# Kernel optimization log

Measured on AMD Instinct MI355X. Metric: run time of the kernel, lower is better.

## Reference

```python
import jax, jax.numpy as jnp
import numpy as np
from jax import lax

DIM = 384
HEADS = 8
HEAD_DIM = DIM // HEADS
EPS = 1e-06


def setup_inputs() -> dict:
    key = jax.random.key(0)
    ks = jax.random.split(key, 16)
    B, N, C = 8, 4096, DIM
    s = 0.02
    inp = {
        "x": jax.random.normal(ks[0], (B, N, C), jnp.float32),
        "wq": jax.random.normal(ks[1], (C, C), jnp.float32) * s,
        "bq": jnp.zeros((C,), jnp.float32),
        "wk": jax.random.normal(ks[2], (C, C), jnp.float32) * s,
        "bk": jnp.zeros((C,), jnp.float32),
        "wv": jax.random.normal(ks[3], (C, C), jnp.float32) * s,
        "bv": jnp.zeros((C,), jnp.float32),
        "wg": jax.random.normal(ks[4], (C, C), jnp.float32) * s,
        "bg": jnp.zeros((C,), jnp.float32),
        "wo": jax.random.normal(ks[5], (C, C), jnp.float32) * s,
        "bo": jnp.zeros((C,), jnp.float32),
        "temperature": jnp.ones((HEADS, 1, 1), jnp.float32),
        "dw_w": jax.random.normal(ks[6], (C, 1, 3, 3), jnp.float32) * s,  # depthwise 3x3
        "dw_b": jnp.zeros((C,), jnp.float32),
        "pw_w": jax.random.normal(ks[7], (C, C), jnp.float32) * s,        # pointwise 1x1
        "pw_b": jnp.zeros((C,), jnp.float32),
    }
    return inp


def _phi(x):
    # exp(x - max) over last dim, numerically stable
    return jnp.exp(x - jnp.max(x, axis=-1, keepdims=True))


def _token_mixer(x, dw_w, dw_b, pw_w, pw_b):
    B, N, C = x.shape
    H = W = int(np.sqrt(N))
    feat = x.transpose(0, 2, 1).reshape(B, C, H, W)
    feat = lax.conv_general_dilated(
        feat, dw_w, window_strides=(1, 1), padding=((1, 1), (1, 1)),
        feature_group_count=C, dimension_numbers=("NCHW", "OIHW", "NCHW"))
    feat = feat + dw_b[None, :, None, None]
    feat = jnp.einsum("bchw,oc->bohw", feat, pw_w) + pw_b[None, :, None, None]
    return feat.reshape(B, C, N).transpose(0, 2, 1)


def reference(x, wq, bq, wk, bk, wv, bv, wg, bg, wo, bo, temperature,
              dw_w, dw_b, pw_w, pw_b):
    B, N, C = x.shape
    residual = x
    x = x + _token_mixer(x, dw_w, dw_b, pw_w, pw_b)

    def heads(y):  # [B,N,C] -> [B,H,N,d]
        return y.reshape(B, N, HEADS, HEAD_DIM).transpose(0, 2, 1, 3)

    q = heads(jnp.einsum("bnc,oc->bno", x, wq) + bq)
    k = heads(jnp.einsum("bnc,oc->bno", x, wk) + bk)
    v = heads(jnp.einsum("bnc,oc->bno", x, wv) + bv)
    g = heads(jnp.einsum("bnc,oc->bno", x, wg) + bg)

    q = _phi(q * temperature[None])       # temperature: [H,1,1] broadcasts over [B,H,N,d]
    k = _phi(k)
    v = v * jax.nn.sigmoid(g)

    kv = jnp.einsum("bhnd,bhne->bhde", k, v)     # [B,H,d,d]
    k_sum = jnp.sum(k, axis=2)                   # [B,H,d]
    num = jnp.einsum("bhnd,bhde->bhne", q, kv)   # [B,H,N,d]
    den = jnp.einsum("bhnd,bhd->bhn", q, k_sum)[..., None] + EPS
    out = num / den

    out = out.transpose(0, 2, 1, 3).reshape(B, N, C)
    out = jnp.einsum("bnc,oc->bno", out, wo) + bo
    return out + 0.0 * residual
```

## Files before the change

kernel.cpp:

```cpp
#include <hip/hip_runtime.h>
#include <math.h>

#define EPSF 1e-6f

typedef __attribute__((ext_vector_type(8))) short bf16x8;
typedef __attribute__((ext_vector_type(4))) float f32x4;
typedef unsigned short u16;
typedef unsigned int u32;

#define MFMA16(a,b,c) __builtin_amdgcn_mfma_f32_16x16x32_bf16((a),(b),(c),0,0,0)

__device__ __forceinline__ u16 f2bf(float f){
  u32 x = __builtin_bit_cast(u32, f);
  u32 r = (x + 0x7fffu + ((x >> 16) & 1u)) >> 16;
  return (u16)r;
}
__device__ __forceinline__ void gll16(const void* g, void* l){
  __builtin_amdgcn_global_load_lds(
      (const __attribute__((address_space(1))) u32*)g,
      (__attribute__((address_space(3))) u32*)l, 16, 0, 0);
}

__global__ __launch_bounds__(256) void k01_prep_dw(
    const float* __restrict__ wq, const float* __restrict__ bq,
    const float* __restrict__ wk, const float* __restrict__ bk,
    const float* __restrict__ wv, const float* __restrict__ bv,
    const float* __restrict__ wg, const float* __restrict__ bg,
    const float* __restrict__ pw_w, const float* __restrict__ wo,
    u16* __restrict__ wpack, u16* __restrict__ pwb, u16* __restrict__ wob,
    float* __restrict__ bpack,
    const float* __restrict__ x, const float* __restrict__ dw_w,
    const float* __restrict__ dw_b, u16* __restrict__ t)
{
  if (blockIdx.x < 3456){
    int idx = blockIdx.x*256 + threadIdx.x;
    const int NW = 1536*384;
    if (idx < NW) {
      int r = idx / 384, c = idx - r*384;
      int h = r / 192, s = (r % 192)/48, d = r % 48;
      const float* w = (s==0)?wq:(s==1)?wk:(s==2)?wv:wg;
      wpack[idx] = f2bf(w[(h*48+d)*384 + c]);
      if (c==0){
        const float* b = (s==0)?bq:(s==1)?bk:(s==2)?bv:bg;
        bpack[r] = b[h*48+d];
      }
    } else if (idx < NW + 147456) {
      pwb[idx - NW] = f2bf(pw_w[idx - NW]);
    } else if (idx < NW + 2*147456) {
      wob[idx - NW - 147456] = f2bf(wo[idx - NW - 147456]);
    }
    return;
  }
  int idx = (blockIdx.x - 3456)*256 + threadIdx.x;
  int c4 = idx % 96; int rest = idx / 96;
  int jg = rest & 15; rest >>= 4;
  int i = rest & 63; int b = rest >> 6;
  int c0 = c4*4, j0 = jg*4;
  float wf[36];
  {
    const float4* wp = (const float4*)(dw_w + c0*9);
    #pragma unroll
    for (int k=0;k<9;k++){
      float4 v = wp[k];
      wf[4*k] = v.x; wf[4*k+1] = v.y; wf[4*k+2] = v.z; wf[4*k+3] = v.w;
    }
  }
  float4 bias = *(const float4*)(dw_b + c0);
  float acc[4][4];
  #pragma unroll
  for (int tk=0;tk<4;tk++){
    acc[tk][0]=bias.x; acc[tk][1]=bias.y; acc[tk][2]=bias.z; acc[tk][3]=bias.w;
  }
  const float* xb = x + ((size_t)b<<12)*384;
  #pragma unroll
  for (int di=-1; di<=1; ++di){
    int ii = i+di; if ((unsigned)ii >= 64u) continue;
    #pragma unroll
    for (int dj=-1; dj<=4; ++dj){
      int jj = j0+dj; if ((unsigned)jj >= 64u) continue;
      float4 xv = *(const float4*)(xb + (size_t)((ii<<6)+jj)*384 + c0);
      #pragma unroll
      for (int tk=0;tk<4;tk++){
        const int dd = dj - tk;
        if (dd < -1 || dd > 1) continue;
        const int tap = (di+1)*3 + (dd+1);
        acc[tk][0] = fmaf(xv.x, wf[0*9+tap], acc[tk][0]);
        acc[tk][1] = fmaf(xv.y, wf[1*9+tap], acc[tk][1]);
        acc[tk][2] = fmaf(xv.z, wf[2*9+tap], acc[tk][2]);
        acc[tk][3] = fmaf(xv.w, wf[3*9+tap], acc[tk][3]);
      }
    }
  }
  int mbase = (b<<12) + (i<<6) + j0;
  #pragma unroll
  for (int tk=0;tk<4;tk++){
    ushort4 o; o.x=f2bf(acc[tk][0]); o.y=f2bf(acc[tk][1]);
    o.z=f2bf(acc[tk][2]); o.w=f2bf(acc[tk][3]);
    *(ushort4*)(t + (size_t)(mbase+tk)*384 + c0) = o;
  }
}

__global__ __launch_bounds__(256) void k2_gemm_pw(
    const u16* __restrict__ t, const u16* __restrict__ pwb,
    const float* __restrict__ x, const float* __restrict__ pw_b,
    u16* __restrict__ xm)
{
  __shared__ __align__(16) u16 smem[32768];
  const int m0 = blockIdx.x * 128;
  const int n0 = blockIdx.y * 128;
  const int tid = threadIdx.x, w = tid>>6, l = tid&63;
  const int lc = l & 15, hi = l >> 4;
  const int osw = ((l&7) ^ (l>>3))*16;
  const f32x4 zf = {0.f,0.f,0.f,0.f};
  f32x4 acc[4][4];
  #pragma unroll
  for (int i=0;i<4;i++)
    #pragma unroll
    for (int j=0;j<4;j++) acc[i][j] = zf;

  const int srow = (w*4)*8 + (l>>3);

  #define K2_STAGE(T, BUF) do {                                            \
    const int k0_ = (T)*64;                                                \
    char* Ab_ = (char*)(smem + (BUF)*8192);                                \
    char* Bb_ = (char*)(smem + 16384 + (BUF)*8192);                        \
    _Pragma("unroll")                                                      \
    for (int i=0;i<4;i++){                                                 \
      gll16((const char*)t   + ((size_t)(m0+srow+i*8)*384 + k0_)*2 + osw,  \
            Ab_ + (w*4+i)*1024);                                           \
      gll16((const char*)pwb + ((size_t)(n0+srow+i*8)*384 + k0_)*2 + osw,  \
            Bb_ + (w*4+i)*1024);                                           \
    }                                                                      \
  } while(0)

  K2_STAGE(0, 0);
  __syncthreads();
  int cur = 0;
  for (int t_=0; t_<6; ++t_){
    if (t_ < 5) K2_STAGE(t_+1, cur^1);
    const u16* As = smem + cur*8192;
    const u16* Bs = smem + 16384 + cur*8192;
    const int wr = (w>>1)*64, wc = (w&1)*64;
    #pragma unroll
    for (int kk=0; kk<64; kk+=32){
      const int sc = (((kk>>3)+hi) ^ (lc&7))*8;
      bf16x8 a[4], bb[4];
      #pragma unroll
      for (int i=0;i<4;i++) a[i]  = *(const bf16x8*)&As[(wr + i*16 + lc)*64 + sc];
      #pragma unroll
      for (int j=0;j<4;j++) bb[j] = *(const bf16x8*)&Bs[(wc + j*16 + lc)*64 + sc];
      #pragma unroll
      for (int i=0;i<4;i++)
        #pragma unroll
        for (int j=0;j<4;j++)
          acc[i][j] = MFMA16(a[i], bb[j], acc[i][j]);
    }
    __syncthreads();
    cur ^= 1;
  }
  #undef K2_STAGE
  const int wr=(w>>1)*64, wc=(w&1)*64;
  #pragma unroll
  for (int j=0;j<4;j++){
    int n = n0 + wc + j*16 + lc;
    float bias = pw_b[n];
    #pragma unroll
    for (int i=0;i<4;i++)
      #pragma unroll
      for (int r=0;r<4;r++){
        int m = m0 + wr + i*16 + hi*4 + r;
        float v = acc[i][j][r] + x[(size_t)m*384 + n] + bias;
        xm[(size_t)m*384 + n] = f2bf(v);
      }
  }
}

__global__ __launch_bounds__(256) void k3_gemm_qkvg(
    const u16* __restrict__ xm, const u16* __restrict__ wpack,
    const float* __restrict__ bpack, const float* __restrict__ temperature,
    u16* __restrict__ qh, float* __restrict__ pkv, float* __restrict__ pks)
{
  __shared__ __align__(16) u16 smem[40960];
  const int m0 = blockIdx.y * 128;
  const int h  = blockIdx.x;
  const int tid = threadIdx.x, w = tid>>6, l = tid&63;
  const int lc = l & 15, hi = l >> 4;
  const int osw = ((l&7) ^ (l>>3))*16;
  const f32x4 zf = {0.f,0.f,0.f,0.f};
  f32x4 acc[2][12];
  #pragma unroll
  for (int i=0;i<2;i++)
    #pragma unroll
    for (int j=0;j<12;j++) acc[i][j] = zf;

  const int arow = (w*4)*8 + (l>>3);
  const int brow = (w*6)*8 + (l>>3);

  #define K3_STAGE(T, BUF) do {                                                \
    const int k0_ = (T)*64;                                                    \
    char* Ab_ = (char*)(smem + (BUF)*8192);                                    \
    char* Bb_ = (char*)(smem + 16384 + (BUF)*12288);                           \
    _Pragma("unroll")                                                          \
    for (int i=0;i<4;i++)                                                      \
      gll16((const char*)xm + ((size_t)(m0+arow+i*8)*384 + k0_)*2 + osw,       \
            Ab_ + (w*4+i)*1024);                                               \
    _Pragma("unroll")                                                          \
    for (int i=0;i<6;i++)                                                      \
      gll16((const char*)wpack + ((size_t)(h*192+brow+i*8)*384 + k0_)*2 + osw, \
            Bb_ + (w*6+i)*1024);                                               \
  } while(0)

  K3_STAGE(0, 0);
  __syncthreads();
  int cur = 0;
  const int rbase = w*32;
  for (int t=0; t<6; ++t){
    if (t < 5) K3_STAGE(t+1, cur^1);
    const u16* Ab = smem + cur*8192;
    const u16* Bb = smem + 16384 + cur*12288;
    #pragma unroll
    for (int kk=0; kk<64; kk+=32){
      const int sc = (((kk>>3)+hi) ^ (lc&7))*8;
      bf16x8 a0 = *(const bf16x8*)&Ab[(rbase +      lc)*64 + sc];
      bf16x8 a1 = *(const bf16x8*)&Ab[(rbase + 16 + lc)*64 + sc];
      #pragma unroll
      for (int j=0;j<12;j++){
        bf16x8 bb = *(const bf16x8*)&Bb[(j*16 + lc)*64 + sc];
        acc[0][j] = MFMA16(a0, bb, acc[0][j]);
        acc[1][j] = MFMA16(a1, bb, acc[1][j]);
      }
    }
    __syncthreads();
    cur ^= 1;
  }
  #undef K3_STAGE

  const float tq = temperature[h];
  const int b = m0 >> 12;
  const int mtile = (m0 >> 7) & 31;
  const size_t bh = (size_t)b*8 + h;
  const int bb0 = h*192;
  float biasq[3], biask[3], biasv[3], biasg[3];
  #pragma unroll
  for (int j=0;j<3;j++){
    biasq[j] = bpack[bb0       + j*16 + lc];
    biask[j] = bpack[bb0 + 48  + j*16 + lc];
    biasv[j] = bpack[bb0 + 96  + j*16 + lc];
    biasg[j] = bpack[bb0 + 144 + j*16 + lc];
  }
  u16* kT = smem;
  u16* vT = smem + 6528;
  float ksp[3] = {0.f, 0.f, 0.f};

  #pragma unroll
  for (int i=0;i<2;i++){
    ushort4 kst[3], vst[3];
    #pragma unroll
    for (int r=0;r<4;r++){
      int m = m0 + w*32 + i*16 + hi*4 + r;
      int n = m & 4095;
      size_t rowq = (bh*4096 + n)*48;
      float q0=(acc[i][0][r]+biasq[0])*tq;
      float q1=(acc[i][1][r]+biasq[1])*tq;
      float q2=(acc[i][2][r]+biasq[2])*tq;
      qh[rowq +      lc] = f2bf(__expf(q0));
      qh[rowq + 16 + lc] = f2bf(__expf(q1));
      qh[rowq + 32 + lc] = f2bf(__expf(q2));
      float s0=acc[i][3][r]+biask[0];
      float s1=acc[i][4][r]+biask[1];
      float s2=acc[i][5][r]+biask[2];
      float mk = fmaxf(s0,fmaxf(s1,s2));
      mk = fmaxf(mk, __shfl_xor(mk,1,64));
      mk = fmaxf(mk, __shfl_xor(mk,2,64));
      mk = fmaxf(mk, __shfl_xor(mk,4,64));
      mk = fmaxf(mk, __shfl_xor(mk,8,64));
      float k0e = __expf(s0-mk), k1e = __expf(s1-mk), k2e = __expf(s2-mk);
      ksp[0] += k0e; ksp[1] += k1e; ksp[2] += k2e;
      u16 kq0=f2bf(k0e), kq1=f2bf(k1e), kq2=f2bf(k2e);
      u16 vq[3];
      #pragma unroll
      for (int j=0;j<3;j++){
        float vv = acc[i][6+j][r] + biasv[j];
        float gg = acc[i][9+j][r] + biasg[j];
        float sg = __builtin_amdgcn_rcpf(1.f + __expf(-gg));
        vq[j] = f2bf(vv*sg);
      }
      if (r==0){ kst[0].x=kq0; kst[1].x=kq1; kst[2].x=kq2; vst[0].x=vq[0]; vst[1].x=vq[1]; vst[2].x=vq[2]; }
      if (r==1){ kst[0].y=kq0; kst[1].y=kq1; kst[2].y=kq2; vst[0].y=vq[0]; vst[1].y=vq[1]; vst[2].y=vq[2]; }
      if (r==2){ kst[0].z=kq0; kst[1].z=kq1; kst[2].z=kq2; vst[0].z=vq[0]; vst[1].z=vq[1]; vst[2].z=vq[2]; }
      if (r==3){ kst[0].w=kq0; kst[1].w=kq1; kst[2].w=kq2; vst[0].w=vq[0]; vst[1].w=vq[1]; vst[2].w=vq[2]; }
    }
    int mb = w*32 + i*16 + hi*4;
    #pragma unroll
    for (int j=0;j<3;j++){
      *(ushort4*)&kT[(j*16+lc)*136 + mb] = kst[j];
      *(ushort4*)&vT[(j*16+lc)*136 + mb] = vst[j];
    }
  }
  __syncthreads();

  bf16x8 af[3], bfv[3];
  #pragma unroll
  for (int da=0;da<3;da++) af[da]  = *(const bf16x8*)&kT[(da*16+lc)*136 + w*32 + hi*8];
  #pragma unroll
  for (int eb=0;eb<3;eb++) bfv[eb] = *(const bf16x8*)&vT[(eb*16+lc)*136 + w*32 + hi*8];
  f32x4 a2[3][3];
  #pragma unroll
  for (int da=0;da<3;da++)
    #pragma unroll
    for (int eb=0;eb<3;eb++)
      a2[da][eb] = MFMA16(af[da], bfv[eb], zf);
  __syncthreads();
  float* pb = (float*)smem + w*2304;
  #pragma unroll
  for (int da=0;da<3;da++)
    #pragma unroll
    for (int eb=0;eb<3;eb++)
      #pragma unroll
      for (int rr=0;rr<4;rr++)
        pb[(da*16 + hi*4 + rr)*48 + eb*16 + lc] = a2[da][eb][rr];
  __syncthreads();
  {
    float* p0 = (float*)smem;
    float* dst = pkv + ((size_t)bh*32 + mtile)*2304;
    for (int u=tid; u<2304; u+=256)
      dst[u] = p0[u] + p0[2304+u] + p0[4608+u] + p0[6912+u];
  }
  #pragma unroll
  for (int j=0;j<3;j++){
    ksp[j] += __shfl_xor(ksp[j],16,64);
    ksp[j] += __shfl_xor(ksp[j],32,64);
  }
  __syncthreads();
  {
    float* kr = (float*)smem;
    if (hi==0){ kr[w*48+lc]=ksp[0]; kr[w*48+16+lc]=ksp[1]; kr[w*48+32+lc]=ksp[2]; }
    __syncthreads();
    if (tid < 48){
      float* ds = pks + ((size_t)bh*32 + mtile)*48;
      ds[tid] = kr[tid] + kr[48+tid] + kr[96+tid] + kr[144+tid];
    }
  }
}

__global__ __launch_bounds__(256) void k5_red(
    const float* __restrict__ pkv, const float* __restrict__ pks,
    u16* __restrict__ kvp)
{
  __shared__ float sm[2304];
  __shared__ float ks[48];
  int bh = blockIdx.x, tid = threadIdx.x;
  const float* base = pkv + (size_t)bh*32*2304;
  for (int u=tid; u<2304; u+=256){
    float v = 0.f;
    #pragma unroll
    for (int m=0;m<32;m++) v += base[(size_t)m*2304 + u];
    sm[u] = v;
  }
  if (tid < 48){
    const float* bk = pks + (size_t)bh*32*48 + tid;
    float v = 0.f;
    #pragma unroll
    for (int m=0;m<32;m++) v += bk[m*48];
    ks[tid] = v;
  }
  __syncthreads();
  for (int u=tid; u<4096; u+=256){
    int e = u >> 6, d = u & 63;
    float v = 0.f;
    if (e < 48 && d < 48)       v = sm[d*48 + e];
    else if (e == 48 && d < 48) v = ks[d];
    kvp[((size_t)bh*64 + e)*64 + d] = f2bf(v);
  }
}

__global__ __launch_bounds__(256) void k6_num(
    const u16* __restrict__ qh, const u16* __restrict__ kvp, u16* __restrict__ ah)
{
  __shared__ __align__(16) u16 As[256*64];
  __shared__ __align__(16) u16 Bs[64*64];
  const int bh = blockIdx.x >> 4, nc = blockIdx.x & 15;
  const int tid = threadIdx.x, w = tid>>6, l = tid&63;
  const int lc = l & 15, hi = l >> 4;
  const f32x4 zf = {0.f,0.f,0.f,0.f};
  const uint4 z4 = {0,0,0,0};
  const u16* gq = qh + ((size_t)bh*4096 + nc*256)*48;
  #pragma unroll
  for (int it=0; it<8; ++it){
    int s = it*256 + tid;
    int row = s>>3, c = s&7, g = c ^ (row&7);
    ((uint4*)As)[s] = (g < 6) ? *(const uint4*)(gq + (size_t)row*48 + g*8) : z4;
  }
  const u16* gk = kvp + (size_t)bh*4096;
  #pragma unroll
  for (int it=0; it<2; ++it){
    int s = it*256 + tid;
    int row = s>>3, c = s&7, g = c ^ (row&7);
    ((uint4*)Bs)[s] = *(const uint4*)(gk + (size_t)row*64 + g*8);
  }
  __syncthreads();
  f32x4 acc[4][4];
  #pragma unroll
  for (int i=0;i<4;i++)
    #pragma unroll
    for (int j=0;j<4;j++) acc[i][j] = zf;
  const int rbase = w*64;
  #pragma unroll
  for (int kk=0; kk<64; kk+=32){
    const int sc = (((kk>>3)+hi) ^ (lc&7))*8;
    bf16x8 a[4], bb[4];
    #pragma unroll
    for (int i=0;i<4;i++) a[i]  = *(const bf16x8*)&As[(rbase + i*16 + lc)*64 + sc];
    #pragma unroll
    for (int j=0;j<4;j++) bb[j] = *(const bf16x8*)&Bs[(j*16 + lc)*64 + sc];
    #pragma unroll
    for (int i=0;i<4;i++)
      #pragma unroll
      for (int j=0;j<4;j++)
        acc[i][j] = MFMA16(a[i], bb[j], acc[i][j]);
  }
  const int b = bh >> 3, h = bh & 7;
  #pragma unroll
  for (int i=0;i<4;i++){
    #pragma unroll
    for (int r=0;r<4;r++){
      float den = __shfl(acc[i][3][r], l & 48, 64) + EPSF;
      float rd = __builtin_amdgcn_rcpf(den);
      int n = nc*256 + rbase + i*16 + hi*4 + r;
      size_t ob = ((size_t)b*4096 + n)*384 + h*48;
      ah[ob +      lc] = f2bf(acc[i][0][r]*rd);
      ah[ob + 16 + lc] = f2bf(acc[i][1][r]*rd);
      ah[ob + 32 + lc] = f2bf(acc[i][2][r]*rd);
    }
  }
}

__global__ __launch_bounds__(256) void k7_gemm_out(
    const u16* __restrict__ ah, const u16* __restrict__ wob,
    const float* __restrict__ bo, float* __restrict__ out)
{
  __shared__ __align__(16) u16 smem[32768];
  const int m0 = blockIdx.x * 128;
  const int n0 = blockIdx.y * 128;
  const int tid = threadIdx.x, w = tid>>6, l = tid&63;
  const int lc = l & 15, hi = l >> 4;
  const int osw = ((l&7) ^ (l>>3))*16;
  const f32x4 zf = {0.f,0.f,0.f,0.f};
  f32x4 acc[4][4];
  #pragma unroll
  for (int i=0;i<4;i++)
    #pragma unroll
    for (int j=0;j<4;j++) acc[i][j] = zf;

  const int srow = (w*4)*8 + (l>>3);

  #define K7_STAGE(T, BUF) do {                                            \
    const int k0_ = (T)*64;                                                \
    char* Ab_ = (char*)(smem + (BUF)*8192);                                \
    char* Bb_ = (char*)(smem + 16384 + (BUF)*8192);                        \
    _Pragma("unroll")                                                      \
    for (int i=0;i<4;i++){                                                 \
      gll16((const char*)ah  + ((size_t)(m0+srow+i*8)*384 + k0_)*2 + osw,  \
            Ab_ + (w*4+i)*1024);                                           \
      gll16((const char*)wob + ((size_t)(n0+srow+i*8)*384 + k0_)*2 + osw,  \
            Bb_ + (w*4+i)*1024);                                           \
    }                                                                      \
  } while(0)

  K7_STAGE(0, 0);
  __syncthreads();
  int cur = 0;
  for (int t_=0; t_<6; ++t_){
    if (t_ < 5) K7_STAGE(t_+1, cur^1);
    const u16* As = smem + cur*8192;
    const u16* Bs = smem + 16384 + cur*8192;
    const int wr = (w>>1)*64, wc = (w&1)*64;
    #pragma unroll
    for (int kk=0; kk<64; kk+=32){
      const int sc = (((kk>>3)+hi) ^ (lc&7))*8;
      bf16x8 a[4], bb[4];
      #pragma unroll
      for (int i=0;i<4;i++) a[i]  = *(const bf16x8*)&As[(wr + i*16 + lc)*64 + sc];
      #pragma unroll
      for (int j=0;j<4;j++) bb[j] = *(const bf16x8*)&Bs[(wc + j*16 + lc)*64 + sc];
      #pragma unroll
      for (int i=0;i<4;i++)
        #pragma unroll
        for (int j=0;j<4;j++)
          acc[i][j] = MFMA16(a[i], bb[j], acc[i][j]);
    }
    __syncthreads();
    cur ^= 1;
  }
  #undef K7_STAGE
  const int wr=(w>>1)*64, wc=(w&1)*64;
  #pragma unroll
  for (int j=0;j<4;j++){
    int n = n0 + wc + j*16 + lc;
    float bias = bo[n];
    #pragma unroll
    for (int i=0;i<4;i++)
      #pragma unroll
      for (int r=0;r<4;r++){
        int m = m0 + wr + i*16 + hi*4 + r;
        out[(size_t)m*384 + n] = acc[i][j][r] + bias;
      }
  }
}

extern "C" void kernel_launch(void* const* d_in, const int* in_sizes, int n_in,
                              void* d_out, int out_size, void* d_ws, size_t ws_size,
                              hipStream_t stream)
{
  const float* x    = (const float*)d_in[0];
  const float* wq   = (const float*)d_in[1];
  const float* bq   = (const float*)d_in[2];
  const float* wk   = (const float*)d_in[3];
  const float* bk   = (const float*)d_in[4];
  const float* wv   = (const float*)d_in[5];
  const float* bv   = (const float*)d_in[6];
  const float* wg   = (const float*)d_in[7];
  const float* bg   = (const float*)d_in[8];
  const float* wo   = (const float*)d_in[9];
  const float* bo   = (const float*)d_in[10];
  const float* temp = (const float*)d_in[11];
  const float* dw_w = (const float*)d_in[12];
  const float* dw_b = (const float*)d_in[13];
  const float* pw_w = (const float*)d_in[14];
  const float* pw_b = (const float*)d_in[15];
  float* out = (float*)d_out;
  char* ws = (char*)d_ws;

  u16*   t       = (u16*)(ws + 0);
  float* pkv     = (float*)(ws + 0);
  float* pks     = (float*)(ws + 18874368);
  u16*   ah      = (u16*)(ws + 0);
  u16*   xm      = (u16*)(ws + 25165824);
  u16*   qh      = (u16*)(ws + 50331648);
  u16*   wpack   = (u16*)(ws + 83886080);
  u16*   pwb     = (u16*)(ws + 85065728);
  u16*   wob     = (u16*)(ws + 85360640);
  float* bpack   = (float*)(ws + 85655552);
  u16*   kvp     = (u16*)(ws + 85661696);

  k01_prep_dw<<<6528, 256, 0, stream>>>(wq,bq,wk,bk,wv,bv,wg,bg,pw_w,wo,
                                        wpack,pwb,wob,bpack,
                                        x, dw_w, dw_b, t);
  k2_gemm_pw<<<dim3(256,3), 256, 0, stream>>>(t, pwb, x, pw_b, xm);
  k3_gemm_qkvg<<<dim3(8,256), 256, 0, stream>>>(xm, wpack, bpack, temp, qh, pkv, pks);
  k5_red<<<64, 256, 0, stream>>>(pkv, pks, kvp);
  k6_num<<<1024, 256, 0, stream>>>(qh, kvp, ah);
  k7_gemm_out<<<dim3(256,3), 256, 0, stream>>>(ah, wob, bo, out);
}
```

Measured before the change: 174.4 us.

## Store attention output head-major via LDS staging and swap k3 grid order

Result: faster. 169.9 us (median of 2 runs) (-2.6%).

```diff
diff --git a/kernel.cpp b/kernel.cpp
--- a/kernel.cpp
+++ b/kernel.cpp
@@ -181,8 +181,8 @@
     u16* __restrict__ qh, float* __restrict__ pkv, float* __restrict__ pks)
 {
   __shared__ __align__(16) u16 smem[40960];
-  const int m0 = blockIdx.y * 128;
-  const int h  = blockIdx.x;
+  const int m0 = blockIdx.x * 128;
+  const int h  = blockIdx.y;
   const int tid = threadIdx.x, w = tid>>6, l = tid&63;
   const int lc = l & 15, hi = l >> 4;
   const int osw = ((l&7) ^ (l>>3))*16;
@@ -375,7 +375,7 @@
 }
 
 __global__ __launch_bounds__(256) void k6_num(
-    const u16* __restrict__ qh, const u16* __restrict__ kvp, u16* __restrict__ ah)
+    const u16* __restrict__ qh, const u16* __restrict__ kvp, u16* __restrict__ ahh)
 {
   __shared__ __align__(16) u16 As[256*64];
   __shared__ __align__(16) u16 Bs[64*64];
@@ -419,24 +419,30 @@
       for (int j=0;j<4;j++)
         acc[i][j] = MFMA16(a[i], bb[j], acc[i][j]);
   }
-  const int b = bh >> 3, h = bh & 7;
+  __syncthreads();
   #pragma unroll
   for (int i=0;i<4;i++){
     #pragma unroll
     for (int r=0;r<4;r++){
       float den = __shfl(acc[i][3][r], l & 48, 64) + EPSF;
       float rd = __builtin_amdgcn_rcpf(den);
-      int n = nc*256 + rbase + i*16 + hi*4 + r;
-      size_t ob = ((size_t)b*4096 + n)*384 + h*48;
-      ah[ob +      lc] = f2bf(acc[i][0][r]*rd);
-      ah[ob + 16 + lc] = f2bf(acc[i][1][r]*rd);
-      ah[ob + 32 + lc] = f2bf(acc[i][2][r]*rd);
-    }
+      int row = rbase + i*16 + hi*4 + r;
+      As[row*48 +      lc] = f2bf(acc[i][0][r]*rd);
+      As[row*48 + 16 + lc] = f2bf(acc[i][1][r]*rd);
+      As[row*48 + 32 + lc] = f2bf(acc[i][2][r]*rd);
+    }
+  }
+  __syncthreads();
+  size_t gab = ((size_t)bh*4096 + nc*256)*48;
+  #pragma unroll
+  for (int it=0; it<6; ++it){
+    int s = it*256 + tid;
+    *(uint4*)(ahh + gab + (size_t)s*8) = *(const uint4*)&As[s*8];
   }
 }
 
 __global__ __launch_bounds__(256) void k7_gemm_out(
-    const u16* __restrict__ ah, const u16* __restrict__ wob,
+    const u16* __restrict__ ahh, const u16* __restrict__ wob,
     const float* __restrict__ bo, float* __restrict__ out)
 {
   __shared__ __align__(16) u16 smem[32768];
@@ -444,7 +450,8 @@
   const int n0 = blockIdx.y * 128;
   const int tid = threadIdx.x, w = tid>>6, l = tid&63;
   const int lc = l & 15, hi = l >> 4;
-  const int osw = ((l&7) ^ (l>>3))*16;
+  const int sw  = (l&7) ^ (l>>3);
+  const int osw = sw*16;
   const f32x4 zf = {0.f,0.f,0.f,0.f};
   f32x4 acc[4][4];
   #pragma unroll
@@ -454,17 +461,21 @@
 
   const int srow = (w*4)*8 + (l>>3);
 
-  #define K7_STAGE(T, BUF) do {                                            \
-    const int k0_ = (T)*64;                                                \
-    char* Ab_ = (char*)(smem + (BUF)*8192);                                \
-    char* Bb_ = (char*)(smem + 16384 + (BUF)*8192);                        \
-    _Pragma("unroll")                                                      \
-    for (int i=0;i<4;i++){                                                 \
-      gll16((const char*)ah  + ((size_t)(m0+srow+i*8)*384 + k0_)*2 + osw,  \
-            Ab_ + (w*4+i)*1024);                                           \
-      gll16((const char*)wob + ((size_t)(n0+srow+i*8)*384 + k0_)*2 + osw,  \
-            Bb_ + (w*4+i)*1024);                                           \
-    }                                                                      \
+  #define K7_STAGE(T, BUF) do {                                              \
+    const int k0_ = (T)*64;                                                  \
+    const int cg_ = k0_/8 + sw;                                              \
+    const int h_  = cg_/6, cc_ = cg_ - h_*6;                                 \
+    char* Ab_ = (char*)(smem + (BUF)*8192);                                  \
+    char* Bb_ = (char*)(smem + 16384 + (BUF)*8192);                          \
+    _Pragma("unroll")                                                        \
+    for (int i=0;i<4;i++){                                                   \
+      int m_ = m0 + srow + i*8;                                              \
+      gll16((const char*)ahh +                                               \
+            ((((size_t)(m_>>12)*8 + h_)*4096 + (m_&4095))*48 + cc_*8)*2,     \
+            Ab_ + (w*4+i)*1024);                                             \
+      gll16((const char*)wob + ((size_t)(n0+srow+i*8)*384 + k0_)*2 + osw,    \
+            Bb_ + (w*4+i)*1024);                                             \
+    }                                                                        \
   } while(0)
 
   K7_STAGE(0, 0);
@@ -534,7 +545,7 @@
   u16*   t       = (u16*)(ws + 0);
   float* pkv     = (float*)(ws + 0);
   float* pks     = (float*)(ws + 18874368);
-  u16*   ah      = (u16*)(ws + 0);
+  u16*   ahh     = (u16*)(ws + 0);
   u16*   xm      = (u16*)(ws + 25165824);
   u16*   qh      = (u16*)(ws + 50331648);
   u16*   wpack   = (u16*)(ws + 83886080);
@@ -547,8 +558,8 @@
                                         wpack,pwb,wob,bpack,
                                         x, dw_w, dw_b, t);
   k2_gemm_pw<<<dim3(256,3), 256, 0, stream>>>(t, pwb, x, pw_b, xm);
-  k3_gemm_qkvg<<<dim3(8,256), 256, 0, stream>>>(xm, wpack, bpack, temp, qh, pkv, pks);
+  k3_gemm_qkvg<<<dim3(256,8), 256, 0, stream>>>(xm, wpack, bpack, temp, qh, pkv, pks);
   k5_red<<<64, 256, 0, stream>>>(pkv, pks, kvp);
-  k6_num<<<1024, 256, 0, stream>>>(qh, kvp, ah);
-  k7_gemm_out<<<dim3(256,3), 256, 0, stream>>>(ah, wob, bo, out);
-}
+  k6_num<<<1024, 256, 0, stream>>>(qh, kvp, ahh);
+  k7_gemm_out<<<dim3(256,3), 256, 0, stream>>>(ahh, wob, bo, out);
+}
```
